# Optimization experiments

Hardware: AMD Instinct MI355X
Metric: run time of the kernel (lower is better)

Reference implementation:

```python
import jax, jax.numpy as jnp
import numpy as np

N = 8192
D = 128
NUM_CLASSES = 100
EPS = 1e-8  # torch CosineSimilarity default eps


def _l2_normalize(x):
    # torch cosine sim divides by max(||x||, eps)
    n = jnp.sqrt(jnp.sum(x * x, axis=-1, keepdims=True))
    return x / jnp.maximum(n, EPS)


def _remove_diag(M):
    # [n, n] -> [n, n-1], dropping the diagonal, no boolean gather needed
    n = M.shape[0]
    return M.reshape(-1)[1:].reshape(n - 1, n + 1)[:, :-1].reshape(n, n - 1)


def setup_inputs() -> dict:
    key = jax.random.key(0)
    k1, k2, k3, k4 = jax.random.split(key, 4)
    inst_embed = jax.random.normal(k1, (N, D), dtype=jnp.float32)
    proxy = jax.random.normal(k2, (N, D), dtype=jnp.float32)
    negative_mask = jax.random.randint(k3, (NUM_CLASSES, N), 0, 2).astype(jnp.float32)
    labels = jax.random.randint(k4, (N,), 0, NUM_CLASSES, dtype=jnp.int64) if jax.config.jax_enable_x64 else jax.random.randint(k4, (N,), 0, NUM_CLASSES, dtype=jnp.int32)
    return {
        "inst_embed": inst_embed,
        "proxy": proxy,
        "negative_mask": negative_mask,
        "labels": labels,
        "temperature": jnp.float32(0.07),
        "margin": jnp.float32(0.0),
    }


def reference(inst_embed, proxy, negative_mask, labels, temperature, margin):
    xn = _l2_normalize(inst_embed)                       # [N, D]
    # pairwise cosine similarity via normalize + matmul (not NxNxD broadcast)
    sim = xn @ xn.T                                      # [N, N]
    instance_zone = jnp.exp((_remove_diag(sim) - margin) / temperature)  # [N, N-1]

    pn = _l2_normalize(proxy)
    inst2proxy_positive = jnp.exp((jnp.sum(xn * pn, axis=-1) - margin) / temperature)  # [N]

    # pos_collected_numerator == True branch
    mask = _remove_diag(negative_mask[labels])           # [N, N-1]
    numerator = jnp.sum(instance_zone * mask, axis=1) + inst2proxy_positive
    denominator = inst2proxy_positive + jnp.sum(instance_zone, axis=1)
    return -jnp.mean(jnp.log(numerator / denominator))
```

## Files before the change

kernel.cpp:

```cpp
#include <hip/hip_runtime.h>
#include <stdint.h>

#define NROWS 8192
#define DD 128
#define EPS 1e-8f
#define LOG2E 1.4426950408889634f

#define SPLIT 16
#define RPB 128
#define NSUB ((NROWS / SPLIT) / 16)
#define NORM_BLOCKS (NROWS / 4)
#define PACK_BLOCKS 3200

typedef __bf16 bf16x8 __attribute__((ext_vector_type(8)));
typedef float f32x4 __attribute__((ext_vector_type(4)));

__device__ __forceinline__ unsigned int f2bf(float f) {
  union { float f; unsigned int u; } v; v.f = f;
  unsigned int u = v.u;
  return (u + 0x7fffu + ((u >> 16) & 1u)) >> 16;
}
__device__ __forceinline__ float bf2f(unsigned int b) {
  union { unsigned int u; float f; } v; v.u = b << 16;
  return v.f;
}
__device__ __forceinline__ bf16x8 u2b(uint4 u) {
  union { uint4 u; bf16x8 b; } v; v.u = u; return v.b;
}

__global__ __launch_bounds__(256) void norm_kernel(
    const float* __restrict__ x, const float* __restrict__ pr,
    const float* __restrict__ nm, const int* __restrict__ lb,
    const float* __restrict__ tptr,
    unsigned short* __restrict__ xnA, unsigned char* __restrict__ xnBt,
    float* __restrict__ p, float* __restrict__ eself, float* __restrict__ mii,
    float* __restrict__ tot, float* __restrict__ msk,
    unsigned int* __restrict__ packed, float* __restrict__ out)
{
  int wave = threadIdx.x >> 6, lane = threadIdx.x & 63;
  int bx = blockIdx.x;

  if (bx >= NORM_BLOCKS) {
    int widx = (bx - NORM_BLOCKS) * 4 + wave;
    int cls = widx >> 7;
    int w64 = widx & 127;
    float v = nm[(size_t)cls * NROWS + w64 * 64 + lane];
    unsigned long long b = __ballot(v != 0.0f);
    if (lane == 0) {
      packed[cls * 256 + w64 * 2] = (unsigned int)b;
      packed[cls * 256 + w64 * 2 + 1] = (unsigned int)(b >> 32);
    }
    return;
  }

  int row = bx * 4 + wave;
  float2 xv = ((const float2*)(x + (size_t)row * DD))[lane];
  float2 pv = ((const float2*)(pr + (size_t)row * DD))[lane];
  float sx = xv.x * xv.x + xv.y * xv.y;
  float sp = pv.x * pv.x + pv.y * pv.y;
  float dp = xv.x * pv.x + xv.y * pv.y;
  #pragma unroll
  for (int m = 1; m < 64; m <<= 1) {
    sx += __shfl_xor(sx, m);
    sp += __shfl_xor(sp, m);
    dp += __shfl_xor(dp, m);
  }
  float inx = 1.f / fmaxf(sqrtf(sx), EPS);
  float inp = 1.f / fmaxf(sqrtf(sp), EPS);
  float s1 = LOG2E / tptr[0];

  unsigned int a0 = f2bf(xv.x * inx * s1), a1 = f2bf(xv.y * inx * s1);
  unsigned int b0 = f2bf(xv.x * inx),      b1 = f2bf(xv.y * inx);
  ((unsigned int*)(xnA + (size_t)row * DD))[lane] = a0 | (a1 << 16);

  {
    int kstep = lane >> 4, qq = (lane >> 2) & 3, pos = lane & 3;
    unsigned int dst = ((unsigned int)(row >> 4)) * 4096u + kstep * 1024u +
                       qq * 256u + (row & 15) * 16u + pos * 4u;
    *(unsigned int*)(xnBt + dst) = b0 | (b1 << 16);
  }

  float ss = bf2f(a0) * bf2f(b0) + bf2f(a1) * bf2f(b1);
  #pragma unroll
  for (int m = 1; m < 64; m <<= 1) ss += __shfl_xor(ss, m);

  if (lane == 0) {
    p[row] = __builtin_amdgcn_exp2f(dp * inx * inp * s1);
    eself[row] = __builtin_amdgcn_exp2f(ss);
    mii[row] = nm[(size_t)lb[row] * NROWS + row];
    tot[row] = 0.f;
    msk[row] = 0.f;
    if (row == 0) out[0] = 0.f;
  }
}

__global__ __launch_bounds__(256, 4) void main_kernel(
    const unsigned short* __restrict__ xnA_u, const unsigned char* __restrict__ xnBt,
    const unsigned int* __restrict__ packed, const int* __restrict__ labels,
    float* __restrict__ tot, float* __restrict__ msk)
{
  int tid = threadIdx.x;
  int wave = tid >> 6, lane = tid & 63;
  int q = lane >> 4, c = lane & 15;
  int rb0 = blockIdx.x * RPB + wave * 16;
  int rb1 = rb0 + 64;

  const bf16x8* xnvA = (const bf16x8*)xnA_u;

  bf16x8 a0[4], a1[4];
  {
    const bf16x8* b = xnvA + (size_t)(rb0 + c) * (DD / 8) + q;
    a0[0] = b[0]; a0[1] = b[4]; a0[2] = b[8]; a0[3] = b[12];
  }
  {
    const bf16x8* b = xnvA + (size_t)(rb1 + c) * (DD / 8) + q;
    a1[0] = b[0]; a1[1] = b[4]; a1[2] = b[8]; a1[3] = b[12];
  }

  int jb = blockIdx.y * (NROWS / SPLIT);

  int r0[4], r1[4];
  unsigned int offP0[4], offP1[4];
  #pragma unroll
  for (int k = 0; k < 4; k++) {
    r0[k] = rb0 + q * 4 + k;
    r1[k] = rb1 + q * 4 + k;
    offP0[k] = (unsigned int)labels[r0[k]] * 256u + (unsigned int)(jb >> 5);
    offP1[k] = (unsigned int)labels[r1[k]] * 256u + (unsigned int)(jb >> 5);
  }
  float t0[4] = {0, 0, 0, 0}, m0[4] = {0, 0, 0, 0};
  float t1[4] = {0, 0, 0, 0}, m1[4] = {0, 0, 0, 0};

  const unsigned char* gB = xnBt + (size_t)(jb >> 4) * 4096 +
                            (unsigned int)(q * 256 + c * 16);

  uint4 nb0 = *(const uint4*)(gB);
  uint4 nb1 = *(const uint4*)(gB + 1024);
  uint4 nb2 = *(const uint4*)(gB + 2048);
  uint4 nb3 = *(const uint4*)(gB + 3072);

  for (int t = 0; t < NSUB; t++) {
    bf16x8 b0 = u2b(nb0), b1 = u2b(nb1), b2 = u2b(nb2), b3 = u2b(nb3);

    if (t + 1 < NSUB) {
      const unsigned char* gb = gB + (size_t)(t + 1) * 4096;
      nb0 = *(const uint4*)(gb);
      nb1 = *(const uint4*)(gb + 1024);
      nb2 = *(const uint4*)(gb + 2048);
      nb3 = *(const uint4*)(gb + 3072);
    }

    unsigned int wc0[4], wc1[4];
    int g = t >> 1;
    #pragma unroll
    for (int k = 0; k < 4; k++) {
      wc0[k] = packed[offP0[k] + g];
      wc1[k] = packed[offP1[k] + g];
    }

    f32x4 acc0 = {0, 0, 0, 0};
    f32x4 acc1 = {0, 0, 0, 0};
    acc0 = __builtin_amdgcn_mfma_f32_16x16x32_bf16(a0[0], b0, acc0, 0, 0, 0);
    acc1 = __builtin_amdgcn_mfma_f32_16x16x32_bf16(a1[0], b0, acc1, 0, 0, 0);
    acc0 = __builtin_amdgcn_mfma_f32_16x16x32_bf16(a0[1], b1, acc0, 0, 0, 0);
    acc1 = __builtin_amdgcn_mfma_f32_16x16x32_bf16(a1[1], b1, acc1, 0, 0, 0);
    acc0 = __builtin_amdgcn_mfma_f32_16x16x32_bf16(a0[2], b2, acc0, 0, 0, 0);
    acc1 = __builtin_amdgcn_mfma_f32_16x16x32_bf16(a1[2], b2, acc1, 0, 0, 0);
    acc0 = __builtin_amdgcn_mfma_f32_16x16x32_bf16(a0[3], b3, acc0, 0, 0, 0);
    acc1 = __builtin_amdgcn_mfma_f32_16x16x32_bf16(a1[3], b3, acc1, 0, 0, 0);

    int pos = (t & 1) * 16 + c;
    #pragma unroll
    for (int k = 0; k < 4; k++) {
      float e = __builtin_amdgcn_exp2f(acc0[k]);
      t0[k] += e;
      m0[k] = fmaf(e, (float)((wc0[k] >> pos) & 1u), m0[k]);
    }
    #pragma unroll
    for (int k = 0; k < 4; k++) {
      float e = __builtin_amdgcn_exp2f(acc1[k]);
      t1[k] += e;
      m1[k] = fmaf(e, (float)((wc1[k] >> pos) & 1u), m1[k]);
    }
  }

  #pragma unroll
  for (int sh = 1; sh < 16; sh <<= 1) {
    #pragma unroll
    for (int k = 0; k < 4; k++) {
      t0[k] += __shfl_xor(t0[k], sh);
      m0[k] += __shfl_xor(m0[k], sh);
      t1[k] += __shfl_xor(t1[k], sh);
      m1[k] += __shfl_xor(m1[k], sh);
    }
  }
  if (c == 0) {
    #pragma unroll
    for (int k = 0; k < 4; k++) {
      atomicAdd(&tot[r0[k]], t0[k]);
      atomicAdd(&msk[r0[k]], m0[k]);
      atomicAdd(&tot[r1[k]], t1[k]);
      atomicAdd(&msk[r1[k]], m1[k]);
    }
  }
}

__global__ __launch_bounds__(256) void loss_kernel(
    const float* __restrict__ p, const float* __restrict__ tot,
    const float* __restrict__ msk, const float* __restrict__ eself,
    const float* __restrict__ mii, float* __restrict__ out)
{
  __shared__ float sd[4];
  int r = blockIdx.x * 256 + threadIdx.x;
  float pi = p[r];
  float es = eself[r];
  float t = tot[r] - es;
  float m = msk[r] - es * mii[r];
  float v = __builtin_amdgcn_logf(pi + t) - __builtin_amdgcn_logf(pi + m);
  float s = v * (1.0f / (LOG2E * (float)NROWS));
  #pragma unroll
  for (int sh = 1; sh < 64; sh <<= 1) s += __shfl_xor(s, sh);
  int wave = threadIdx.x >> 6, lane = threadIdx.x & 63;
  if (lane == 0) sd[wave] = s;
  __syncthreads();
  if (threadIdx.x == 0) atomicAdd(out, sd[0] + sd[1] + sd[2] + sd[3]);
}

extern "C" void kernel_launch(void* const* d_in, const int* in_sizes, int n_in,
                              void* d_out, int out_size, void* d_ws, size_t ws_size,
                              hipStream_t stream) {
  const float* x  = (const float*)d_in[0];
  const float* pr = (const float*)d_in[1];
  const float* nm = (const float*)d_in[2];
  const int*   lb = (const int*)d_in[3];
  const float* tp = (const float*)d_in[4];

  char* ws = (char*)d_ws;
  unsigned short* xnA = (unsigned short*)ws;
  unsigned char* xnBt = (unsigned char*)(xnA + (size_t)NROWS * DD);
  float* p     = (float*)(xnBt + (size_t)NROWS * DD * 2);
  float* tot   = p + NROWS;
  float* msk   = tot + NROWS;
  float* eself = msk + NROWS;
  float* miiv  = eself + NROWS;
  unsigned int* packed = (unsigned int*)(miiv + NROWS);
  float* out = (float*)d_out;

  norm_kernel<<<NORM_BLOCKS + PACK_BLOCKS, 256, 0, stream>>>(
      x, pr, nm, lb, tp, xnA, xnBt, p, eself, miiv, tot, msk, packed, out);
  main_kernel<<<dim3(NROWS / RPB, SPLIT), 256, 0, stream>>>(xnA, xnBt, packed,
                                                            lb, tot, msk);
  loss_kernel<<<NROWS / 256, 256, 0, stream>>>(p, tot, msk, eself, miiv, out);
}
```

Baseline: 109.9 us.

## Stage B tiles into double-buffered LDS via global_load_lds shared across waves

The main kernel now copies 64-column B tiles into a double-buffered shared-memory region using direct global-to-LDS loads, cooperatively across the four waves. Each wave then reads its B operands from LDS instead of every wave loading the same B data from global memory. Mask words are fetched as uint2 once per tile. This is meant to cut redundant global and L2 traffic and improve overlap, at the cost of LDS usage and a block-wide barrier per tile.

```diff
diff --git a/kernel.cpp b/kernel.cpp
--- a/kernel.cpp
+++ b/kernel.cpp
@@ -8,12 +8,16 @@
 
 #define SPLIT 16
 #define RPB 128
-#define NSUB ((NROWS / SPLIT) / 16)
+#define TCOLS 64
+#define TBYTES (TCOLS * 256)
+#define NT ((NROWS / SPLIT) / TCOLS)
 #define NORM_BLOCKS (NROWS / 4)
 #define PACK_BLOCKS 3200
 
 typedef __bf16 bf16x8 __attribute__((ext_vector_type(8)));
 typedef float f32x4 __attribute__((ext_vector_type(4)));
+typedef __attribute__((address_space(1))) unsigned int as1_u32;
+typedef __attribute__((address_space(3))) unsigned int as3_u32;
 
 __device__ __forceinline__ unsigned int f2bf(float f) {
   union { float f; unsigned int u; } v; v.f = f;
@@ -23,9 +27,6 @@
 __device__ __forceinline__ float bf2f(unsigned int b) {
   union { unsigned int u; float f; } v; v.u = b << 16;
   return v.f;
-}
-__device__ __forceinline__ bf16x8 u2b(uint4 u) {
-  union { uint4 u; bf16x8 b; } v; v.u = u; return v.b;
 }
 
 __global__ __launch_bounds__(256) void norm_kernel(
@@ -99,6 +100,7 @@
     const unsigned int* __restrict__ packed, const int* __restrict__ labels,
     float* __restrict__ tot, float* __restrict__ msk)
 {
+  __shared__ unsigned char lds[2][TBYTES];
   int tid = threadIdx.x;
   int wave = tid >> 6, lane = tid & 63;
   int q = lane >> 4, c = lane & 15;
@@ -131,57 +133,70 @@
   float t0[4] = {0, 0, 0, 0}, m0[4] = {0, 0, 0, 0};
   float t1[4] = {0, 0, 0, 0}, m1[4] = {0, 0, 0, 0};
 
-  const unsigned char* gB = xnBt + (size_t)(jb >> 4) * 4096 +
-                            (unsigned int)(q * 256 + c * 16);
-
-  uint4 nb0 = *(const uint4*)(gB);
-  uint4 nb1 = *(const uint4*)(gB + 1024);
-  uint4 nb2 = *(const uint4*)(gB + 2048);
-  uint4 nb3 = *(const uint4*)(gB + 3072);
-
-  for (int t = 0; t < NSUB; t++) {
-    bf16x8 b0 = u2b(nb0), b1 = u2b(nb1), b2 = u2b(nb2), b3 = u2b(nb3);
-
-    if (t + 1 < NSUB) {
-      const unsigned char* gb = gB + (size_t)(t + 1) * 4096;
-      nb0 = *(const uint4*)(gb);
-      nb1 = *(const uint4*)(gb + 1024);
-      nb2 = *(const uint4*)(gb + 2048);
-      nb3 = *(const uint4*)(gb + 3072);
-    }
-
-    unsigned int wc0[4], wc1[4];
-    int g = t >> 1;
+  const unsigned char* gW = xnBt + (size_t)(jb >> 4) * 4096 +
+                            (unsigned int)(wave * 4096 + lane * 16);
+  unsigned int ldsW = (unsigned int)(wave * 4096);
+
+  auto stage = [&](int t, int b) {
+    const unsigned char* g = gW + (unsigned int)t * (unsigned int)TBYTES;
+    unsigned char* d = lds[b] + ldsW;
+    #pragma unroll
+    for (int i = 0; i < 4; i++) {
+      __builtin_amdgcn_global_load_lds((const as1_u32*)(g + i * 1024),
+                                       (as3_u32*)(d + i * 1024), 16, 0, 0);
+    }
+  };
+
+  stage(0, 0);
+  __syncthreads();
+
+  for (int t = 0; t < NT; t++) {
+    if (t + 1 < NT) stage(t + 1, (t + 1) & 1);
+
+    uint2 wA0[4], wA1[4];
     #pragma unroll
     for (int k = 0; k < 4; k++) {
-      wc0[k] = packed[offP0[k] + g];
-      wc1[k] = packed[offP1[k] + g];
-    }
-
-    f32x4 acc0 = {0, 0, 0, 0};
-    f32x4 acc1 = {0, 0, 0, 0};
-    acc0 = __builtin_amdgcn_mfma_f32_16x16x32_bf16(a0[0], b0, acc0, 0, 0, 0);
-    acc1 = __builtin_amdgcn_mfma_f32_16x16x32_bf16(a1[0], b0, acc1, 0, 0, 0);
-    acc0 = __builtin_amdgcn_mfma_f32_16x16x32_bf16(a0[1], b1, acc0, 0, 0, 0);
-    acc1 = __builtin_amdgcn_mfma_f32_16x16x32_bf16(a1[1], b1, acc1, 0, 0, 0);
-    acc0 = __builtin_amdgcn_mfma_f32_16x16x32_bf16(a0[2], b2, acc0, 0, 0, 0);
-    acc1 = __builtin_amdgcn_mfma_f32_16x16x32_bf16(a1[2], b2, acc1, 0, 0, 0);
-    acc0 = __builtin_amdgcn_mfma_f32_16x16x32_bf16(a0[3], b3, acc0, 0, 0, 0);
-    acc1 = __builtin_amdgcn_mfma_f32_16x16x32_bf16(a1[3], b3, acc1, 0, 0, 0);
-
-    int pos = (t & 1) * 16 + c;
-    #pragma unroll
-    for (int k = 0; k < 4; k++) {
-      float e = __builtin_amdgcn_exp2f(acc0[k]);
-      t0[k] += e;
-      m0[k] = fmaf(e, (float)((wc0[k] >> pos) & 1u), m0[k]);
-    }
-    #pragma unroll
-    for (int k = 0; k < 4; k++) {
-      float e = __builtin_amdgcn_exp2f(acc1[k]);
-      t1[k] += e;
-      m1[k] = fmaf(e, (float)((wc1[k] >> pos) & 1u), m1[k]);
-    }
+      wA0[k] = *(const uint2*)&packed[offP0[k] + 2 * t];
+      wA1[k] = *(const uint2*)&packed[offP1[k] + 2 * t];
+    }
+
+    const unsigned char* buf = lds[t & 1] + (unsigned int)(lane * 16);
+    #pragma unroll
+    for (int s = 0; s < 4; s++) {
+      const unsigned char* sb = buf + s * 4096;
+      bf16x8 b0 = *(const bf16x8*)(sb);
+      bf16x8 b1 = *(const bf16x8*)(sb + 1024);
+      bf16x8 b2 = *(const bf16x8*)(sb + 2048);
+      bf16x8 b3 = *(const bf16x8*)(sb + 3072);
+
+      f32x4 acc0 = {0, 0, 0, 0};
+      f32x4 acc1 = {0, 0, 0, 0};
+      acc0 = __builtin_amdgcn_mfma_f32_16x16x32_bf16(a0[0], b0, acc0, 0, 0, 0);
+      acc1 = __builtin_amdgcn_mfma_f32_16x16x32_bf16(a1[0], b0, acc1, 0, 0, 0);
+      acc0 = __builtin_amdgcn_mfma_f32_16x16x32_bf16(a0[1], b1, acc0, 0, 0, 0);
+      acc1 = __builtin_amdgcn_mfma_f32_16x16x32_bf16(a1[1], b1, acc1, 0, 0, 0);
+      acc0 = __builtin_amdgcn_mfma_f32_16x16x32_bf16(a0[2], b2, acc0, 0, 0, 0);
+      acc1 = __builtin_amdgcn_mfma_f32_16x16x32_bf16(a1[2], b2, acc1, 0, 0, 0);
+      acc0 = __builtin_amdgcn_mfma_f32_16x16x32_bf16(a0[3], b3, acc0, 0, 0, 0);
+      acc1 = __builtin_amdgcn_mfma_f32_16x16x32_bf16(a1[3], b3, acc1, 0, 0, 0);
+
+      int pos = (s & 1) * 16 + c;
+      #pragma unroll
+      for (int k = 0; k < 4; k++) {
+        unsigned int w = (s < 2) ? wA0[k].x : wA0[k].y;
+        float e = __builtin_amdgcn_exp2f(acc0[k]);
+        t0[k] += e;
+        m0[k] = fmaf(e, (float)((w >> pos) & 1u), m0[k]);
+      }
+      #pragma unroll
+      for (int k = 0; k < 4; k++) {
+        unsigned int w = (s < 2) ? wA1[k].x : wA1[k].y;
+        float e = __builtin_amdgcn_exp2f(acc1[k]);
+        t1[k] += e;
+        m1[k] = fmaf(e, (float)((w >> pos) & 1u), m1[k]);
+      }
+    }
+    __syncthreads();
   }
 
   #pragma unroll
```

After: 119.5 us. 8.7% more time.
